# Kernel tuning notes

Measured on AMD Instinct MI355X. Metric: run time of the kernel, lower is better.

The kernel has to match this reference:

```python
import jax, jax.numpy as jnp
import numpy as np
import math

N, H, D_MODEL = 2048, 16, 2048
D_K = D_MODEL // H
D_FF = 4 * D_MODEL
EPS = 1e-5


def _layernorm(x, alpha, beta):
    # torch: mean/var over dim=1 (=feature dim for 2D input), unbiased=False
    m = jnp.mean(x, axis=1, keepdims=True)
    v = jnp.var(x, axis=1, keepdims=True)
    return (x - m) / jnp.sqrt(v + EPS) * alpha + beta


def setup_inputs() -> dict:
    key = jax.random.key(0)
    ks = jax.random.split(key, 12)
    s = 0.02  # weight init scale
    return {
        "X": jax.random.normal(ks[0], (N, D_MODEL), jnp.float32),
        "Wq": jax.random.normal(ks[1], (H, D_MODEL, D_K), jnp.float32) * s,
        "bq": jax.random.normal(ks[2], (H, D_K), jnp.float32) * s,
        "Wk": jax.random.normal(ks[3], (H, D_MODEL, D_K), jnp.float32) * s,
        "bk": jax.random.normal(ks[4], (H, D_K), jnp.float32) * s,
        "Wv": jax.random.normal(ks[5], (H, D_MODEL, D_K), jnp.float32) * s,
        "bv": jax.random.normal(ks[6], (H, D_K), jnp.float32) * s,
        "alpha1": jnp.ones((N, D_MODEL), jnp.float32),
        "beta1": jnp.zeros((N, D_MODEL), jnp.float32),
        "W1": jax.random.normal(ks[7], (D_MODEL, D_FF), jnp.float32) * s,
        "b1": jax.random.normal(ks[8], (D_FF,), jnp.float32) * s,
        "W2": jax.random.normal(ks[9], (D_FF, D_MODEL), jnp.float32) * s,
        "b2": jax.random.normal(ks[10], (D_MODEL,), jnp.float32) * s,
        "alpha2": jnp.ones((N, D_MODEL), jnp.float32),
        "beta2": jnp.zeros((N, D_MODEL), jnp.float32),
    }


def reference(X, Wq, bq, Wk, bk, Wv, bv, alpha1, beta1, W1, b1, W2, b2, alpha2, beta2):
    # --- Multi-headed self-attention (h per-head linears fused as stacked weights) ---
    Q = jnp.einsum('nd,hdk->hnk', X, Wq) + bq[:, None, :]  # (H, N, D_K)
    K = jnp.einsum('nd,hdk->hnk', X, Wk) + bk[:, None, :]
    V = jnp.einsum('nd,hdk->hnk', X, Wv) + bv[:, None, :]
    scores = jnp.einsum('hnk,hmk->hnm', Q, K) / math.sqrt(D_K)  # (H, N, N)
    A = jax.nn.softmax(scores, axis=-1)  # softmax over keys (torch dim=1 of 2D)
    O = jnp.einsum('hnm,hmk->hnk', A, V)  # (H, N, D_K)
    attn = jnp.transpose(O, (1, 0, 2)).reshape(N, D_MODEL)  # concat heads on dim=1
    # --- Add & Norm 1 (dropout is identity at inference) ---
    h1 = _layernorm(X + attn, alpha1, beta1)
    # --- FFN ---
    ffn = jnp.maximum(h1 @ W1 + b1, 0.0) @ W2 + b2
    # --- Add & Norm 2 ---
    return _layernorm(h1 + ffn, alpha2, beta2)
```

## Files before the change

### kernel.cpp

```cpp
#include <hip/hip_runtime.h>
#include <hip/hip_bf16.h>

#define N_TOK 2048
#define DMODEL 2048
#define NH 16
#define DK 128
#define DFF 8192

typedef __attribute__((ext_vector_type(8))) short short8;
typedef __attribute__((ext_vector_type(4))) short s16x4;
typedef __attribute__((ext_vector_type(4))) float f32x4;

__device__ __forceinline__ short f2bf(float f) {
    unsigned int x = __builtin_bit_cast(unsigned int, f);
    unsigned int r = (x + 0x7fffu + ((x >> 16) & 1u)) >> 16;
    return (short)r;
}

__global__ __launch_bounds__(256) void cast_f32_bf16(const float* __restrict__ in,
                                                     short* __restrict__ out, int n8) {
    int i = blockIdx.x * 256 + threadIdx.x;
    if (i >= n8) return;
    const float4* p = (const float4*)in + (size_t)i * 2;
    float4 a = p[0], b = p[1];
    short8 o;
    o[0] = f2bf(a.x); o[1] = f2bf(a.y); o[2] = f2bf(a.z); o[3] = f2bf(a.w);
    o[4] = f2bf(b.x); o[5] = f2bf(b.y); o[6] = f2bf(b.z); o[7] = f2bf(b.w);
    *(short8*)(out + (size_t)i * 8) = o;
}

template <typename TIN>
__global__ __launch_bounds__(256) void transpose_cast(const TIN* __restrict__ in,
                                                      short* __restrict__ out,
                                                      int R, int C, long sIn, long sOut) {
    __shared__ float t[64][65];
    in  += (long)blockIdx.z * sIn;
    out += (long)blockIdx.z * sOut;
    int tx = threadIdx.x & 63, ty = threadIdx.x >> 6;
    long r0 = (long)blockIdx.y * 64, c0 = (long)blockIdx.x * 64;
    for (int i = 0; i < 16; i++) {
        int r = ty + i * 4;
        t[r][tx] = (float)in[(r0 + r) * (long)C + c0 + tx];
    }
    __syncthreads();
    for (int i = 0; i < 16; i++) {
        int r = ty + i * 4;
        out[(c0 + r) * (long)R + r0 + tx] = f2bf(t[tx][r]);
    }
}

__device__ __forceinline__ void gld_lds16(const void* g, void* l) {
    __builtin_amdgcn_global_load_lds(
        (const __attribute__((address_space(1))) void*)g,
        (__attribute__((address_space(3))) void*)l, 16, 0, 0);
}

#define VM8 asm volatile("s_waitcnt vmcnt(8)" ::: "memory")
#define VM4 asm volatile("s_waitcnt vmcnt(4)" ::: "memory")
#define VM0 asm volatile("s_waitcnt vmcnt(0)" ::: "memory")
#define VMNONE ((void)0)

#define PHASE(BUF, MH, NH, STAGE_STMT, VMSTMT)                                  \
  {                                                                             \
    if (NH == 0) {                                                              \
      _Pragma("unroll") for (int mp = 0; mp < 4; mp++)                          \
        _Pragma("unroll") for (int kk = 0; kk < 2; kk++) {                      \
          int rowA = wr * 128 + (MH) * 64 + mp * 16 + fr;                       \
          af[mp][kk] = *(const short8*)((const char*)lds + (BUF) * 65536 +      \
                         rowA * 128 + (((kk * 4 + fq) ^ (rowA & 7)) << 4));     \
        }                                                                       \
    }                                                                           \
    _Pragma("unroll") for (int np = 0; np < 2; np++)                            \
      _Pragma("unroll") for (int kk = 0; kk < 2; kk++) {                        \
        int rowB = wc * 64 + (NH) * 32 + np * 16 + fr;                          \
        bf[np][kk] = *(const short8*)((const char*)lds + (BUF) * 65536 + 32768 +\
                       rowB * 128 + (((kk * 4 + fq) ^ (rowB & 7)) << 4));       \
      }                                                                         \
    STAGE_STMT;                                                                 \
    __builtin_amdgcn_s_barrier();                                               \
    asm volatile("s_waitcnt lgkmcnt(0)" ::: "memory");                          \
    __builtin_amdgcn_sched_barrier(0);                                          \
    __builtin_amdgcn_s_setprio(1);                                              \
    _Pragma("unroll") for (int mp = 0; mp < 4; mp++)                            \
      _Pragma("unroll") for (int np = 0; np < 2; np++)                          \
        _Pragma("unroll") for (int kk = 0; kk < 2; kk++)                        \
          acc[(MH) * 4 + mp][(NH) * 2 + np] =                                   \
              __builtin_amdgcn_mfma_f32_16x16x32_bf16(                          \
                  af[mp][kk], bf[np][kk], acc[(MH) * 4 + mp][(NH) * 2 + np],    \
                  0, 0, 0);                                                     \
    __builtin_amdgcn_s_setprio(0);                                              \
    VMSTMT;                                                                     \
    __builtin_amdgcn_sched_barrier(0);                                          \
    __builtin_amdgcn_s_barrier();                                               \
    __builtin_amdgcn_sched_barrier(0);                                          \
  }

template <int MODE>
__global__ __launch_bounds__(512, 2) void gemm256(const short* __restrict__ A,
                                                  const short* __restrict__ Bt,
                                                  void* __restrict__ Cv,
                                                  const float* __restrict__ b0,
                                                  const float* __restrict__ b1,
                                                  const float* __restrict__ b2,
                                                  int Ktot, int TM) {
    __shared__ short lds[65536];
    const int tid = threadIdx.x, lane = tid & 63, w = tid >> 6;
    const int T = gridDim.x, bid = blockIdx.x;
    const int vbid = (bid & 7) * (T >> 3) + (bid >> 3);
    const int mt = vbid % TM;
    const int rest = vbid / TM;
    int nt = rest, z = 0;
    if (MODE == 2) { nt = rest & 7; z = rest >> 3; }
    const long brow = (long)mt * 256, bcol = (long)nt * 256;
    const short* Ab = A + (MODE == 2 ? (long)z * 2048 : 0);
    const short* Bb = Bt + (MODE == 2 ? (long)z * 2048 : 0);

    auto stageA = [&](int kt, int buf, int mh) {
#pragma unroll
        for (int j = 0; j < 2; j++) {
            int row = mh * 64 + j * 128 + (tid >> 3);
            int g = (lane & 7) ^ (row & 7);
            gld_lds16((const char*)(Ab + (brow + row) * (long)Ktot + (long)kt * 64) + g * 16,
                      (char*)lds + buf * 65536 + mh * 8192 + j * 16384 + w * 1024 + lane * 16);
        }
    };
    auto stageB = [&](int kt, int buf, int nh) {
#pragma unroll
        for (int j = 0; j < 2; j++) {
            int s = 2 * j + (w >> 2);
            int rin = (w & 3) * 8 + (lane >> 3);
            int row = s * 64 + nh * 32 + rin;
            int g = (lane & 7) ^ (row & 7);
            gld_lds16((const char*)(Bb + (bcol + row) * (long)Ktot + (long)kt * 64) + g * 16,
                      (char*)lds + buf * 65536 + 32768 + j * 16384 + (w >> 2) * 8192 +
                          nh * 4096 + (w & 3) * 1024 + lane * 16);
        }
    };

    const int wr = w >> 2, wc = w & 3;
    const int fr = lane & 15, fq = lane >> 4;
    f32x4 acc[8][4] = {};
    short8 af[4][2], bf[2][2];

    stageA(0, 0, 0); stageB(0, 0, 0); stageA(0, 0, 1); stageB(0, 0, 1);
    stageA(1, 1, 0); stageB(1, 1, 0);
    VM8;
    __builtin_amdgcn_s_barrier();

    for (int i = 0; i < 15; i++) {
        const int t1 = 2 * i + 1, kn = 2 * i + 2;
        PHASE(0, 0, 0, { stageA(t1, 1, 1); stageB(t1, 1, 1); }, VM8)
        PHASE(0, 0, 1, { stageA(kn, 0, 0); }, VMNONE)
        PHASE(0, 1, 0, {}, VMNONE)
        PHASE(0, 1, 1, { stageB(kn, 0, 0); }, VM8)
        PHASE(1, 0, 0, { stageA(kn, 0, 1); stageB(kn, 0, 1); }, VM8)
        PHASE(1, 0, 1, { stageA(kn + 1, 1, 0); }, VMNONE)
        PHASE(1, 1, 0, {}, VMNONE)
        PHASE(1, 1, 1, { stageB(kn + 1, 1, 0); }, VM8)
    }
    PHASE(0, 0, 0, { stageA(31, 1, 1); stageB(31, 1, 1); }, VM8)
    PHASE(0, 0, 1, {}, VMNONE)
    PHASE(0, 1, 0, {}, VMNONE)
    PHASE(0, 1, 1, {}, VM4)
    PHASE(1, 0, 0, {}, VM0)
    PHASE(1, 0, 1, {}, VMNONE)
    PHASE(1, 1, 0, {}, VMNONE)
    PHASE(1, 1, 1, {}, VMNONE)

    const long crow0 = brow + wr * 128, ccol0 = bcol + wc * 64;
#pragma unroll
    for (int n = 0; n < 4; n++) {
        const long col = ccol0 + (n >> 1) * 32 + (n & 1) * 16 + fr;
        float bval = 0.f;
        if (MODE == 0) {
            const float* bp = (col >> 11) == 0 ? b0 : (col >> 11) == 1 ? b1 : b2;
            bval = bp[col & 2047];
        } else if (MODE == 1) bval = b0[col];
#pragma unroll
        for (int m = 0; m < 8; m++) {
#pragma unroll
            for (int r = 0; r < 4; r++) {
                const long row = crow0 + (m >> 2) * 64 + (m & 3) * 16 + fq * 4 + r;
                float v = acc[m][n][r] + bval;
                if (MODE == 0) {
                    const long slab = col >> 7;
                    ((short*)Cv)[slab * (2048L * 128) + row * 128 + (col & 127)] = f2bf(v);
                } else if (MODE == 1) {
                    ((short*)Cv)[row * 8192 + col] = f2bf(fmaxf(v, 0.f));
                } else {
                    ((float*)Cv)[(long)z * (2048L * 2048) + row * 2048 + col] = v;
                }
            }
        }
    }
}

__global__ __launch_bounds__(512, 2) void attn_flash(const short* __restrict__ Q,
                                                     const short* __restrict__ Kc,
                                                     const short* __restrict__ VT,
                                                     float* __restrict__ O) {
    __shared__ short lds[32768];
    const int tid = threadIdx.x, lane = tid & 63, w = tid >> 6;
    const int bid = blockIdx.x;
    const int vid = (bid & 7) * 32 + (bid >> 3);
    const int h = vid >> 4, qt = vid & 15;
    const int fr = lane & 15, fq = lane >> 4;
    const long qbase = (long)qt * 128 + w * 16;
    const short* Qh = Q  + (long)h * N_TOK * DK;
    const short* Kh = Kc + (long)h * N_TOK * DK;
    const short* Vh = VT + (long)h * DK * N_TOK;
    short* Pw = lds + 24576 + w * 1024;

    short8 qf[4];
#pragma unroll
    for (int c = 0; c < 4; c++)
        qf[c] = *(const short8*)(Qh + (qbase + fr) * DK + c * 32 + fq * 8);

    float mrow = -1e30f, lrow = 0.f;
    f32x4 oacc[8] = {};
    const float C1 = 0.08838834764831845f * 1.4426950408889634f;

    int wr_off[4], rd_off[2];
#pragma unroll
    for (int jc = 0; jc < 4; jc++)
        wr_off[jc] = (fr * 64 + jc * 16 + fq * 4) ^ ((fr & 7) << 3);
#pragma unroll
    for (int kc = 0; kc < 2; kc++)
        rd_off[kc] = (fr * 64 + kc * 32 + fq * 8) ^ ((fr & 7) << 3);
    int colKb[4], colVb[2];
#pragma unroll
    for (int c = 0; c < 4; c++) colKb[c] = (c * 64 + fq * 16) ^ ((fr & 7) << 4);
#pragma unroll
    for (int kc = 0; kc < 2; kc++) colVb[kc] = (kc * 64 + fq * 16) ^ ((fr & 7) << 4);

    auto stageK = [&](int kvt, int buf) {
        const char* Kg = (const char*)(Kh + (long)kvt * 64 * DK);
        char* Kd = (char*)(lds + buf * 8192);
#pragma unroll
        for (int i = 0; i < 2; i++) {
            int a = (w * 2 + i) * 1024 + (lane << 4);
            int src = a ^ (((a >> 8) & 7) << 4);
            gld_lds16(Kg + src, Kd + (w * 2 + i) * 1024);
        }
    };
    auto stageV = [&](int kvt) {
        char* Vd = (char*)(lds + 16384);
#pragma unroll
        for (int i = 0; i < 2; i++) {
            int a = (w * 2 + i) * 1024 + (lane << 4);
            int row = a >> 7;
            int inner = (a & 127) ^ ((row & 7) << 4);
            const char* src = (const char*)Vh + ((long)row * N_TOK + (long)kvt * 64) * 2 + inner;
            gld_lds16(src, Vd + (w * 2 + i) * 1024);
        }
    };

    const int NT = N_TOK / 64;
    stageK(0, 0);
    __syncthreads();

    for (int t = 0; t < NT; t++) {
        const int cur = t & 1;
        stageV(t);
        if (t + 1 < NT) stageK(t + 1, cur ^ 1);

        const char* Kcb = (const char*)(lds + cur * 8192);
        f32x4 s[4] = {};
#pragma unroll
        for (int jc = 0; jc < 4; jc++) {
            const char* rb = Kcb + (jc * 16 + fr) * 256;
#pragma unroll
            for (int c = 0; c < 4; c++) {
                short8 kf = *(const short8*)(rb + colKb[c]);
                s[jc] = __builtin_amdgcn_mfma_f32_16x16x32_bf16(kf, qf[c], s[jc], 0, 0, 0);
            }
        }

        float tm = -1e30f;
#pragma unroll
        for (int jc = 0; jc < 4; jc++)
#pragma unroll
            for (int r = 0; r < 4; r++) tm = fmaxf(tm, s[jc][r]);
        tm = fmaxf(tm, __shfl_xor(tm, 16));
        tm = fmaxf(tm, __shfl_xor(tm, 32));
        float nm = fmaxf(mrow, tm);
        float resc = exp2f(C1 * (mrow - nm));
        mrow = nm;
        float sum = 0.f;
#pragma unroll
        for (int jc = 0; jc < 4; jc++)
#pragma unroll
            for (int r = 0; r < 4; r++) {
                float p = exp2f(C1 * (s[jc][r] - nm));
                s[jc][r] = p;
                sum += p;
            }
        sum += __shfl_xor(sum, 16);
        sum += __shfl_xor(sum, 32);
        lrow = lrow * resc + sum;
#pragma unroll
        for (int f = 0; f < 8; f++)
#pragma unroll
            for (int r = 0; r < 4; r++) oacc[f][r] *= resc;

#pragma unroll
        for (int jc = 0; jc < 4; jc++) {
            s16x4 pk;
            pk[0] = f2bf(s[jc][0]); pk[1] = f2bf(s[jc][1]);
            pk[2] = f2bf(s[jc][2]); pk[3] = f2bf(s[jc][3]);
            *(s16x4*)(Pw + wr_off[jc]) = pk;
        }
        short8 pa[2];
#pragma unroll
        for (int kc = 0; kc < 2; kc++)
            pa[kc] = *(const short8*)(Pw + rd_off[kc]);

        __syncthreads();

        const char* Vcb = (const char*)(lds + 16384);
#pragma unroll
        for (int f = 0; f < 8; f++) {
            const char* rb = Vcb + (f * 16 + fr) * 128;
#pragma unroll
            for (int kc = 0; kc < 2; kc++) {
                short8 vf = *(const short8*)(rb + colVb[kc]);
                oacc[f] = __builtin_amdgcn_mfma_f32_16x16x32_bf16(vf, pa[kc], oacc[f], 0, 0, 0);
            }
        }
        __syncthreads();
    }

    const float inv = 1.f / lrow;
    const long row = qbase + fr;
#pragma unroll
    for (int f = 0; f < 8; f++) {
        float4 o;
        o.x = oacc[f][0] * inv; o.y = oacc[f][1] * inv;
        o.z = oacc[f][2] * inv; o.w = oacc[f][3] * inv;
        *(float4*)(O + row * (long)DMODEL + h * DK + f * 16 + fq * 4) = o;
    }
}

template <bool WBF>
__global__ __launch_bounds__(256) void add_ln(const float* __restrict__ A,
                                              const float* __restrict__ B,
                                              const float* __restrict__ alpha,
                                              const float* __restrict__ beta,
                                              float* __restrict__ out,
                                              short* __restrict__ outbf) {
    const int row = blockIdx.x, t = threadIdx.x;
    const long base = (long)row * DMODEL;
    float4 va[2], vb[2];
    float s = 0.f, q = 0.f;
#pragma unroll
    for (int i = 0; i < 2; i++) {
        long off = base + (long)(t + i * 256) * 4;
        va[i] = *(const float4*)(A + off);
        vb[i] = *(const float4*)(B + off);
        float x0 = va[i].x + vb[i].x, x1 = va[i].y + vb[i].y;
        float x2 = va[i].z + vb[i].z, x3 = va[i].w + vb[i].w;
        s += x0 + x1 + x2 + x3;
        q += x0 * x0 + x1 * x1 + x2 * x2 + x3 * x3;
    }
#pragma unroll
    for (int o = 1; o < 64; o <<= 1) { s += __shfl_xor(s, o); q += __shfl_xor(q, o); }
    __shared__ float red[8];
    if ((t & 63) == 0) { red[t >> 6] = s; red[4 + (t >> 6)] = q; }
    __syncthreads();
    s = red[0] + red[1] + red[2] + red[3];
    q = red[4] + red[5] + red[6] + red[7];
    const float mean = s * (1.f / DMODEL);
    const float var = q * (1.f / DMODEL) - mean * mean;
    const float rstd = rsqrtf(var + 1e-5f);
#pragma unroll
    for (int i = 0; i < 2; i++) {
        long off = base + (long)(t + i * 256) * 4;
        float4 al = *(const float4*)(alpha + off);
        float4 be = *(const float4*)(beta + off);
        float x[4] = { va[i].x + vb[i].x, va[i].y + vb[i].y, va[i].z + vb[i].z, va[i].w + vb[i].w };
        float a[4] = { al.x, al.y, al.z, al.w };
        float b[4] = { be.x, be.y, be.z, be.w };
#pragma unroll
        for (int j = 0; j < 4; j++) {
            float o2 = (x[j] - mean) * rstd * a[j] + b[j];
            out[off + j] = o2;
            if (WBF) outbf[off + j] = f2bf(o2);
        }
    }
}

__global__ __launch_bounds__(256) void add_ln2_red(const float* __restrict__ H1,
                                                   const float* __restrict__ F4,
                                                   const float* __restrict__ b2,
                                                   const float* __restrict__ alpha,
                                                   const float* __restrict__ beta,
                                                   float* __restrict__ out) {
    const int row = blockIdx.x, t = threadIdx.x;
    const long base = (long)row * DMODEL;
    const long SL = (long)N_TOK * DMODEL;
    float x[8];
    float s = 0.f, q = 0.f;
#pragma unroll
    for (int i = 0; i < 2; i++) {
        long off = base + (long)(t + i * 256) * 4;
        int col = (t + i * 256) * 4;
        float4 a  = *(const float4*)(H1 + off);
        float4 f0 = *(const float4*)(F4 + off);
        float4 f1 = *(const float4*)(F4 + off + SL);
        float4 f2 = *(const float4*)(F4 + off + 2 * SL);
        float4 f3 = *(const float4*)(F4 + off + 3 * SL);
        float4 bb = *(const float4*)(b2 + col);
        x[i * 4 + 0] = a.x + f0.x + f1.x + f2.x + f3.x + bb.x;
        x[i * 4 + 1] = a.y + f0.y + f1.y + f2.y + f3.y + bb.y;
        x[i * 4 + 2] = a.z + f0.z + f1.z + f2.z + f3.z + bb.z;
        x[i * 4 + 3] = a.w + f0.w + f1.w + f2.w + f3.w + bb.w;
#pragma unroll
        for (int j = 0; j < 4; j++) { s += x[i * 4 + j]; q += x[i * 4 + j] * x[i * 4 + j]; }
    }
#pragma unroll
    for (int o = 1; o < 64; o <<= 1) { s += __shfl_xor(s, o); q += __shfl_xor(q, o); }
    __shared__ float red[8];
    if ((t & 63) == 0) { red[t >> 6] = s; red[4 + (t >> 6)] = q; }
    __syncthreads();
    s = red[0] + red[1] + red[2] + red[3];
    q = red[4] + red[5] + red[6] + red[7];
    const float mean = s * (1.f / DMODEL);
    const float var = q * (1.f / DMODEL) - mean * mean;
    const float rstd = rsqrtf(var + 1e-5f);
#pragma unroll
    for (int i = 0; i < 2; i++) {
        long off = base + (long)(t + i * 256) * 4;
        float4 al = *(const float4*)(alpha + off);
        float4 be = *(const float4*)(beta + off);
        float a[4] = { al.x, al.y, al.z, al.w };
        float b[4] = { be.x, be.y, be.z, be.w };
#pragma unroll
        for (int j = 0; j < 4; j++)
            out[off + j] = (x[i * 4 + j] - mean) * rstd * a[j] + b[j];
    }
}

extern "C" void kernel_launch(void* const* d_in, const int* in_sizes, int n_in,
                              void* d_out, int out_size, void* d_ws, size_t ws_size,
                              hipStream_t stream) {
    const float* X      = (const float*)d_in[0];
    const float* Wq     = (const float*)d_in[1];
    const float* bq     = (const float*)d_in[2];
    const float* Wk     = (const float*)d_in[3];
    const float* bk     = (const float*)d_in[4];
    const float* Wv     = (const float*)d_in[5];
    const float* bv     = (const float*)d_in[6];
    const float* alpha1 = (const float*)d_in[7];
    const float* beta1  = (const float*)d_in[8];
    const float* W1     = (const float*)d_in[9];
    const float* b1     = (const float*)d_in[10];
    const float* W2     = (const float*)d_in[11];
    const float* b2     = (const float*)d_in[12];
    const float* alpha2 = (const float*)d_in[13];
    const float* beta2  = (const float*)d_in[14];
    float* out = (float*)d_out;

    char* ws = (char*)d_ws;
    size_t off = 0;
    auto alloc = [&](size_t bytes) -> void* {
        void* p = ws + off;
        off += (bytes + 255) & ~(size_t)255;
        return p;
    };
    short* XBF   = (short*)alloc(2048UL * 2048 * 2);
    short* WQKVT = (short*)alloc(48UL * 128 * 2048 * 2);
    short* W1T   = (short*)alloc(8192UL * 2048 * 2);
    short* W2T   = (short*)alloc(2048UL * 8192 * 2);
    short* QKV   = (short*)alloc(48UL * 2048 * 128 * 2);
    short* VT    = (short*)alloc(16UL * 128 * 2048 * 2);
    float* ATTN  = (float*)alloc(2048UL * 2048 * 4);
    float* H1    = (float*)alloc(2048UL * 2048 * 4);
    short* H1BF  = (short*)alloc(2048UL * 2048 * 2);
    short* G     = (short*)alloc(2048UL * 8192 * 2);
    float* F4 = (float*)XBF;

    cast_f32_bf16<<<2048, 256, 0, stream>>>(X, XBF, 2048 * 2048 / 8);
    transpose_cast<float><<<dim3(2, 32, 16), 256, 0, stream>>>(Wq, WQKVT,                    2048, 128, 2048L * 128, 128L * 2048);
    transpose_cast<float><<<dim3(2, 32, 16), 256, 0, stream>>>(Wk, WQKVT + 16L * 128 * 2048, 2048, 128, 2048L * 128, 128L * 2048);
    transpose_cast<float><<<dim3(2, 32, 16), 256, 0, stream>>>(Wv, WQKVT + 32L * 128 * 2048, 2048, 128, 2048L * 128, 128L * 2048);
    transpose_cast<float><<<dim3(128, 32, 1), 256, 0, stream>>>(W1, W1T, 2048, 8192, 0, 0);
    transpose_cast<float><<<dim3(32, 128, 1), 256, 0, stream>>>(W2, W2T, 8192, 2048, 0, 0);

    gemm256<0><<<192, 512, 0, stream>>>(XBF, WQKVT, QKV, bq, bk, bv, 2048, 8);

    transpose_cast<__hip_bfloat16><<<dim3(2, 32, 16), 256, 0, stream>>>(
        (const __hip_bfloat16*)(QKV + 32L * 2048 * 128), VT, 2048, 128, 2048L * 128, 128L * 2048);

    attn_flash<<<256, 512, 0, stream>>>(QKV, QKV + 16L * 2048 * 128, VT, ATTN);

    add_ln<true><<<2048, 256, 0, stream>>>(X, ATTN, alpha1, beta1, H1, H1BF);

    gemm256<1><<<256, 512, 0, stream>>>(H1BF, W1T, G, b1, nullptr, nullptr, 2048, 8);
    gemm256<2><<<256, 512, 0, stream>>>(G, W2T, F4, nullptr, nullptr, nullptr, 8192, 8);

    add_ln2_red<<<2048, 256, 0, stream>>>(H1, F4, b2, alpha2, beta2, out);
}
```

Measured before the change: 383.6 us.

## Double-buffer B fragments in registers and reorder GEMM stage schedule

The 256-tile GEMM main loop now keeps both halves of the B fragments in registers (bf gains an extra dimension), so the B fragments are read from LDS only in the first two phases of each buffer rather than once per phase. Phases that reuse a fragment skip the LDS read. The global-to-LDS staging schedule is also reordered: the prologue stages two full k-tiles, and stage issues plus vmcnt waits are redistributed so a k-tile finishes loading before the buffer is reused. The goal is fewer LDS reads and better overlap of loads with MFMA, at the cost of more VGPRs, which under launch_bounds(512,2) could spill or pressure occupancy.

Measured after the change: 378.8 us. Within noise of the previous version (-1.3%).

```diff
diff --git a/kernel.cpp b/kernel.cpp
--- a/kernel.cpp
+++ b/kernel.cpp
@@ -56,13 +56,12 @@
 }
 
 #define VM8 asm volatile("s_waitcnt vmcnt(8)" ::: "memory")
-#define VM4 asm volatile("s_waitcnt vmcnt(4)" ::: "memory")
 #define VM0 asm volatile("s_waitcnt vmcnt(0)" ::: "memory")
 #define VMNONE ((void)0)
 
-#define PHASE(BUF, MH, NH, STAGE_STMT, VMSTMT)                                  \
+#define PHASE(BUF, MH, NHI, RA, RBNH, STAGE_STMT, VMSTMT)                       \
   {                                                                             \
-    if (NH == 0) {                                                              \
+    if (RA) {                                                                   \
       _Pragma("unroll") for (int mp = 0; mp < 4; mp++)                          \
         _Pragma("unroll") for (int kk = 0; kk < 2; kk++) {                      \
           int rowA = wr * 128 + (MH) * 64 + mp * 16 + fr;                       \
@@ -70,12 +69,15 @@
                          rowA * 128 + (((kk * 4 + fq) ^ (rowA & 7)) << 4));     \
         }                                                                       \
     }                                                                           \
-    _Pragma("unroll") for (int np = 0; np < 2; np++)                            \
-      _Pragma("unroll") for (int kk = 0; kk < 2; kk++) {                        \
-        int rowB = wc * 64 + (NH) * 32 + np * 16 + fr;                          \
-        bf[np][kk] = *(const short8*)((const char*)lds + (BUF) * 65536 + 32768 +\
-                       rowB * 128 + (((kk * 4 + fq) ^ (rowB & 7)) << 4));       \
-      }                                                                         \
+    if ((RBNH) < 2) {                                                           \
+      _Pragma("unroll") for (int np = 0; np < 2; np++)                          \
+        _Pragma("unroll") for (int kk = 0; kk < 2; kk++) {                      \
+          int rowB = wc * 64 + (RBNH) * 32 + np * 16 + fr;                      \
+          bf[(RBNH) & 1][np][kk] =                                              \
+              *(const short8*)((const char*)lds + (BUF) * 65536 + 32768 +       \
+                  rowB * 128 + (((kk * 4 + fq) ^ (rowB & 7)) << 4));            \
+        }                                                                       \
+    }                                                                           \
     STAGE_STMT;                                                                 \
     __builtin_amdgcn_s_barrier();                                               \
     asm volatile("s_waitcnt lgkmcnt(0)" ::: "memory");                          \
@@ -84,9 +86,9 @@
     _Pragma("unroll") for (int mp = 0; mp < 4; mp++)                            \
       _Pragma("unroll") for (int np = 0; np < 2; np++)                          \
         _Pragma("unroll") for (int kk = 0; kk < 2; kk++)                        \
-          acc[(MH) * 4 + mp][(NH) * 2 + np] =                                   \
+          acc[(MH) * 4 + mp][(NHI) * 2 + np] =                                  \
               __builtin_amdgcn_mfma_f32_16x16x32_bf16(                          \
-                  af[mp][kk], bf[np][kk], acc[(MH) * 4 + mp][(NH) * 2 + np],    \
+                  af[mp][kk], bf[NHI][np][kk], acc[(MH) * 4 + mp][(NHI) * 2 + np],\
                   0, 0, 0);                                                     \
     __builtin_amdgcn_s_setprio(0);                                              \
     VMSTMT;                                                                     \
@@ -140,32 +142,32 @@
     const int wr = w >> 2, wc = w & 3;
     const int fr = lane & 15, fq = lane >> 4;
     f32x4 acc[8][4] = {};
-    short8 af[4][2], bf[2][2];
-
-    stageA(0, 0, 0); stageB(0, 0, 0); stageA(0, 0, 1); stageB(0, 0, 1);
-    stageA(1, 1, 0); stageB(1, 1, 0);
+    short8 af[4][2], bf[2][2][2];
+
+    stageA(0, 0, 0); stageB(0, 0, 0); stageB(0, 0, 1); stageA(0, 0, 1);
+    stageA(1, 1, 0); stageB(1, 1, 0); stageB(1, 1, 1); stageA(1, 1, 1);
     VM8;
     __builtin_amdgcn_s_barrier();
 
     for (int i = 0; i < 15; i++) {
-        const int t1 = 2 * i + 1, kn = 2 * i + 2;
-        PHASE(0, 0, 0, { stageA(t1, 1, 1); stageB(t1, 1, 1); }, VM8)
-        PHASE(0, 0, 1, { stageA(kn, 0, 0); }, VMNONE)
-        PHASE(0, 1, 0, {}, VMNONE)
-        PHASE(0, 1, 1, { stageB(kn, 0, 0); }, VM8)
-        PHASE(1, 0, 0, { stageA(kn, 0, 1); stageB(kn, 0, 1); }, VM8)
-        PHASE(1, 0, 1, { stageA(kn + 1, 1, 0); }, VMNONE)
-        PHASE(1, 1, 0, {}, VMNONE)
-        PHASE(1, 1, 1, { stageB(kn + 1, 1, 0); }, VM8)
-    }
-    PHASE(0, 0, 0, { stageA(31, 1, 1); stageB(31, 1, 1); }, VM8)
-    PHASE(0, 0, 1, {}, VMNONE)
-    PHASE(0, 1, 0, {}, VMNONE)
-    PHASE(0, 1, 1, {}, VM4)
-    PHASE(1, 0, 0, {}, VM0)
-    PHASE(1, 0, 1, {}, VMNONE)
-    PHASE(1, 1, 0, {}, VMNONE)
-    PHASE(1, 1, 1, {}, VMNONE)
+        const int kn = 2 * i + 2;
+        PHASE(0, 0, 0, 1, 0, {}, VMNONE)
+        PHASE(0, 0, 1, 0, 1, { stageA(kn, 0, 0); stageB(kn, 0, 0); }, VMNONE)
+        PHASE(0, 1, 0, 1, 2, { stageB(kn, 0, 1); }, VMNONE)
+        PHASE(0, 1, 1, 0, 2, { stageA(kn, 0, 1); }, VM8)
+        PHASE(1, 0, 0, 1, 0, {}, VMNONE)
+        PHASE(1, 0, 1, 0, 1, { stageA(kn + 1, 1, 0); stageB(kn + 1, 1, 0); }, VMNONE)
+        PHASE(1, 1, 0, 1, 2, { stageB(kn + 1, 1, 1); }, VMNONE)
+        PHASE(1, 1, 1, 0, 2, { stageA(kn + 1, 1, 1); }, VM8)
+    }
+    PHASE(0, 0, 0, 1, 0, {}, VMNONE)
+    PHASE(0, 0, 1, 0, 1, {}, VMNONE)
+    PHASE(0, 1, 0, 1, 2, {}, VMNONE)
+    PHASE(0, 1, 1, 0, 2, {}, VM0)
+    PHASE(1, 0, 0, 1, 0, {}, VMNONE)
+    PHASE(1, 0, 1, 0, 1, {}, VMNONE)
+    PHASE(1, 1, 0, 1, 2, {}, VMNONE)
+    PHASE(1, 1, 1, 0, 2, {}, VMNONE)
 
     const long crow0 = brow + wr * 128, ccol0 = bcol + wc * 64;
 #pragma unroll
```
